# Kernel tuning notes

Measured on AMD Instinct MI355X. Metric: run time of the kernel, lower is better.

Reference implementation:

```python
import jax, jax.numpy as jnp
import numpy as np

N, IN, HID, H, OUT, G = 2048, 128, 128, 4, 10, 8
NEG_SLOPE = 0.2
THRESHOLD = 0.0


def setup_inputs() -> dict:
    key = jax.random.key(0)
    ks = jax.random.split(key, 18)
    s = 0.05
    return {
        "x": jax.random.normal(ks[0], (N, IN), jnp.float32),
        "attn_tensor": jax.random.normal(ks[1], (12, N, N), jnp.float32),
        "batch_idx": jnp.sort(jax.random.randint(ks[2], (N,), 0, G)),
        "conv_w": jax.random.normal(ks[3], (12,), jnp.float32) * s,
        "conv_b": jnp.zeros((), jnp.float32),
        "W1": jax.random.normal(ks[4], (IN, H * HID), jnp.float32) * s,
        "att_src1": jax.random.normal(ks[5], (H, HID), jnp.float32) * s,
        "att_dst1": jax.random.normal(ks[6], (H, HID), jnp.float32) * s,
        "att_edge1": jax.random.normal(ks[7], (H, HID), jnp.float32) * s,
        "We1": jax.random.normal(ks[8], (H * HID,), jnp.float32) * s,
        "b1": jnp.zeros((H * HID,), jnp.float32),
        "W2": jax.random.normal(ks[9], (H * HID, HID), jnp.float32) * s,
        "att_src2": jax.random.normal(ks[10], (1, HID), jnp.float32) * s,
        "att_dst2": jax.random.normal(ks[11], (1, HID), jnp.float32) * s,
        "att_edge2": jax.random.normal(ks[12], (1, HID), jnp.float32) * s,
        "We2": jax.random.normal(ks[13], (HID,), jnp.float32) * s,
        "b2": jnp.zeros((HID,), jnp.float32),
        "fc_w": jax.random.normal(ks[14], (HID, OUT), jnp.float32) * s,
        "fc_b": jnp.zeros((OUT,), jnp.float32),
    }


def gat_layer(x, adj, eattr, W, a_src, a_dst, a_edge, We, b, heads, out_ch):
    n = x.shape[0]
    h = (x @ W).reshape(n, heads, out_ch)            # [N,H,C]
    s_src = jnp.einsum('nhc,hc->nh', h, a_src)       # alpha contribution of source node
    s_dst = jnp.einsum('nhc,hc->nh', h, a_dst)       # alpha contribution of target node
    c_e = jnp.einsum('hc,hc->h', a_edge, We.reshape(heads, out_ch))  # scalar edge coeff per head
    # logits[s,t,h] for message s -> t (edge (s,t) means agg_mat[s,t] > thr)
    logits = s_src[:, None, :] + s_dst[None, :, :] + eattr[:, :, None] * c_e[None, None, :]
    logits = jnp.where(logits >= 0, logits, NEG_SLOPE * logits)  # leaky_relu(0.2)
    logits = jnp.where(adj[:, :, None], logits, -1e9)
    alpha = jax.nn.softmax(logits, axis=0)           # segment softmax over sources per target
    out = jnp.einsum('sth,shc->thc', alpha, h).reshape(n, heads * out_ch)
    return out + b


def reference(x, attn_tensor, batch_idx, conv_w, conv_b,
              W1, att_src1, att_dst1, att_edge1, We1, b1,
              W2, att_src2, att_dst2, att_edge2, We2, b2,
              fc_w, fc_b):
    # 1x1 conv over 12 attention channels -> dense [N,N] aggregated matrix
    agg = jnp.einsum('c,cst->st', conv_w, attn_tensor) + conv_b
    eye = jnp.eye(N, dtype=bool)
    mask_off = (agg > THRESHOLD) & (~eye)            # PyG GATConv removes then re-adds self loops
    # self-loop edge_attr = mean of incoming edge attrs per target (fill_value='mean')
    cnt = mask_off.sum(axis=0)
    mean_attr = jnp.where(mask_off, agg, 0.0).sum(axis=0) / jnp.maximum(cnt, 1)
    eattr = jnp.where(mask_off, agg, 0.0) + jnp.diag(mean_attr)
    adj = mask_off | eye

    h = gat_layer(x, adj, eattr, W1, att_src1, att_dst1, att_edge1, We1, b1, H, HID)
    h = jax.nn.relu(h)
    h = gat_layer(h, adj, eattr, W2, att_src2, att_dst2, att_edge2, We2, b2, 1, HID)

    sums = jax.ops.segment_sum(h, batch_idx, num_segments=G)
    counts = jax.ops.segment_sum(jnp.ones((N,), h.dtype), batch_idx, num_segments=G)
    pooled = sums / jnp.maximum(counts, 1.0)[:, None]  # global_mean_pool
    return jax.nn.log_softmax(pooled @ fc_w + fc_b, axis=1)
```

## Files before the change

### kernel.cpp

```cpp
#include <hip/hip_runtime.h>
#include <hip/hip_bf16.h>
#include <math.h>

#define NN 2048
#define NEG_SLOPE 0.2f

typedef __attribute__((ext_vector_type(8))) short bf16x8;
typedef __attribute__((ext_vector_type(4))) float f32x4;

static __device__ inline short f2bf(float x) {
  union { float f; unsigned u; } v;
  v.f = x;
  unsigned r = v.u + 0x7fffu + ((v.u >> 16) & 1u);
  return (short)(r >> 16);
}

__global__ __launch_bounds__(256) void k_pre(
    const float* __restrict__ attn, const float* __restrict__ conv_w,
    const float* __restrict__ conv_b, const float* __restrict__ W1,
    const float* __restrict__ W2, const float* __restrict__ ae1,
    const float* __restrict__ We1, const float* __restrict__ ae2,
    const float* __restrict__ We2, float* __restrict__ aggT,
    float* __restrict__ ssum_part, float* __restrict__ scnt_part,
    __hip_bfloat16* __restrict__ w1t, __hip_bfloat16* __restrict__ w2t,
    float* __restrict__ ce) {
  const int b = blockIdx.x;
  const int tid = threadIdx.x;
  if (b < 1024) {
    __shared__ float tile[64][68];
    const int t0 = (b & 31) * 64;
    const int s0 = (b >> 5) * 64;
    const int sl = tid >> 4;
    const int t4 = (tid & 15) * 4;
    float w[12];
#pragma unroll
    for (int c = 0; c < 12; ++c) w[c] = conv_w[c];
    const float cb = conv_b[0];
    f32x4 acc[4];
#pragma unroll
    for (int k = 0; k < 4; ++k) acc[k] = (f32x4){cb, cb, cb, cb};
    for (int c = 0; c < 12; ++c) {
      const float* base =
          attn + (size_t)c * NN * NN + (size_t)(s0 + sl) * NN + t0 + t4;
#pragma unroll
      for (int k = 0; k < 4; ++k)
        acc[k] += w[c] * *(const f32x4*)(base + (size_t)k * 16 * NN);
    }
#pragma unroll
    for (int k = 0; k < 4; ++k) *(f32x4*)&tile[sl + 16 * k][t4] = acc[k];
    __syncthreads();
    const int tl = tid >> 2;
    const int sq = (tid & 3) * 16;
    const int tglob = t0 + tl;
    float* orow = aggT + (size_t)tglob * NN + s0 + sq;
    float psum = 0.f, pcnt = 0.f;
#pragma unroll
    for (int g = 0; g < 4; ++g) {
      f32x4 v = {tile[sq + 4 * g][tl], tile[sq + 4 * g + 1][tl],
                 tile[sq + 4 * g + 2][tl], tile[sq + 4 * g + 3][tl]};
      *(f32x4*)(orow + 4 * g) = v;
#pragma unroll
      for (int j = 0; j < 4; ++j) {
        int sglob = s0 + sq + 4 * g + j;
        bool m = (v[j] > 0.f) && (sglob != tglob);
        psum += m ? v[j] : 0.f;
        pcnt += m ? 1.f : 0.f;
      }
    }
    psum += __shfl_down(psum, 1); psum += __shfl_down(psum, 2);
    pcnt += __shfl_down(pcnt, 1); pcnt += __shfl_down(pcnt, 2);
    if ((tid & 3) == 0) {
      ssum_part[(b >> 5) * NN + tglob] = psum;
      scnt_part[(b >> 5) * NN + tglob] = pcnt;
    }
  } else if (b < 1056) {
#pragma unroll
    for (int k = 0; k < 8; ++k) {
      int o = (b - 1024) * 2048 + k * 256 + tid;
      ((short*)w1t)[o] = f2bf(W1[(o & 127) * 512 + (o >> 7)]);
    }
  } else if (b < 1088) {
#pragma unroll
    for (int k = 0; k < 8; ++k) {
      int o = (b - 1056) * 2048 + k * 256 + tid;
      ((short*)w2t)[o] = f2bf(W2[(o & 511) * 128 + (o >> 9)]);
    }
  } else {
    const int lane = tid & 63;
    const int wv = tid >> 6;
    float q1 = ae1[wv * 128 + lane] * We1[wv * 128 + lane] +
               ae1[wv * 128 + 64 + lane] * We1[wv * 128 + 64 + lane];
    for (int off = 32; off; off >>= 1) q1 += __shfl_down(q1, off);
    if (lane == 0) ce[wv] = q1;
    float q2 = ae2[lane] * We2[lane] + ae2[64 + lane] * We2[64 + lane];
    for (int off = 32; off; off >>= 1) q2 += __shfl_down(q2, off);
    if (tid == 0) ce[4] = q2;
  }
}

__global__ __launch_bounds__(256) void k_gemm1(
    const float* __restrict__ x, const __hip_bfloat16* __restrict__ w1t,
    const float* __restrict__ asrc1, const float* __restrict__ adst1,
    __hip_bfloat16* __restrict__ hTsw1, float* __restrict__ sspart1,
    float* __restrict__ sdpart1) {
  const int tid = threadIdx.x;
  const int w = (int)blockIdx.x * 4 + (tid >> 6);
  const int lane = tid & 63, row = lane & 15, kg = lane >> 4;
  const int mb = w >> 4, nb = w & 15;
  const int m0 = mb * 16, n0 = nb * 32;
  const float* axrow = x + (size_t)(m0 + row) * 128 + kg * 8;
  f32x4 acc[2];
#pragma unroll
  for (int f = 0; f < 2; ++f) acc[f] = (f32x4){0.f, 0.f, 0.f, 0.f};
#pragma unroll
  for (int ks = 0; ks < 4; ++ks) {
    f32x4 xa = *(const f32x4*)(axrow + ks * 32);
    f32x4 xb = *(const f32x4*)(axrow + ks * 32 + 4);
    bf16x8 Af = {f2bf(xa[0]), f2bf(xa[1]), f2bf(xa[2]), f2bf(xa[3]),
                 f2bf(xb[0]), f2bf(xb[1]), f2bf(xb[2]), f2bf(xb[3])};
#pragma unroll
    for (int f = 0; f < 2; ++f) {
      bf16x8 Bf = *(const bf16x8*)(w1t + (size_t)(n0 + f * 16 + row) * 128 +
                                   kg * 8 + ks * 32);
      acc[f] = __builtin_amdgcn_mfma_f32_16x16x32_bf16(Af, Bf, acc[f], 0, 0, 0);
    }
  }
  const int h = nb >> 2;
  float as[2], ad[2];
#pragma unroll
  for (int f = 0; f < 2; ++f) {
    int ch = (n0 + f * 16 + row) & 127;
    as[f] = asrc1[h * 128 + ch];
    ad[f] = adst1[h * 128 + ch];
  }
  float ps[4] = {0.f, 0.f, 0.f, 0.f}, pd[4] = {0.f, 0.f, 0.f, 0.f};
#pragma unroll
  for (int f = 0; f < 2; ++f)
#pragma unroll
    for (int r = 0; r < 4; ++r) {
      ps[r] += acc[f][r] * as[f];
      pd[r] += acc[f][r] * ad[f];
    }
#pragma unroll
  for (int m = 1; m < 16; m <<= 1) {
#pragma unroll
    for (int r = 0; r < 4; ++r) {
      ps[r] += __shfl_xor(ps[r], m);
      pd[r] += __shfl_xor(pd[r], m);
    }
  }
  if (row == 0) {
#pragma unroll
    for (int r = 0; r < 4; ++r) {
      int node = m0 + kg * 4 + r;
      sspart1[nb * NN + node] = ps[r];
      sdpart1[nb * NN + node] = pd[r];
    }
  }
#pragma unroll
  for (int f = 0; f < 2; ++f) {
    const int cbi = nb * 2 + f;
    short4 ct;
    ct.x = f2bf(acc[f][0]); ct.y = f2bf(acc[f][1]);
    ct.z = f2bf(acc[f][2]); ct.w = f2bf(acc[f][3]);
    size_t a4 = (size_t)cbi * (NN * 16) +
                (size_t)(((m0 >> 3) + (kg >> 1)) * 128 + row * 8 + (kg & 1) * 4);
    *(short4*)((short*)hTsw1 + a4) = ct;
  }
}

__global__ __launch_bounds__(256) void k_attn1(
    const float* __restrict__ aggT, const __hip_bfloat16* __restrict__ hTsw1,
    const float* __restrict__ sspart1, const float* __restrict__ sdpart1,
    const float* __restrict__ ssum_part, const float* __restrict__ scnt_part,
    const float* __restrict__ ce_all, const float* __restrict__ b1,
    __hip_bfloat16* __restrict__ feat1b) {
  const int tid = threadIdx.x;
  const int t0 = (int)(blockIdx.x >> 2) * 16;
  const int h = (int)(blockIdx.x & 3u);
  __shared__ float ss_sh[2048];
  __shared__ float red[4][16][128];
  __shared__ float den_sh[4][16];
  for (int i = tid; i < 2048; i += 256)
    ss_sh[i] = sspart1[(4 * h + 0) * NN + i] + sspart1[(4 * h + 1) * NN + i] +
               sspart1[(4 * h + 2) * NN + i] + sspart1[(4 * h + 3) * NN + i];
  __syncthreads();
  const int lane = tid & 63, w = tid >> 6, row = lane & 15, kg = lane >> 4;
  const int sbeg = w * 512;
  const int tRow = t0 + row;
  const float* arow = aggT + (size_t)tRow * NN;
  float msum = 0.f, mcnt = 0.f;
#pragma unroll
  for (int q = 0; q < 32; ++q) {
    msum += ssum_part[q * NN + tRow];
    mcnt += scnt_part[q * NN + tRow];
  }
  const float ma_t = msum / fmaxf(mcnt, 1.f);
  const float ce = ce_all[h];
  const float sd_t = sdpart1[(4 * h + 0) * NN + tRow] +
                     sdpart1[(4 * h + 1) * NN + tRow] +
                     sdpart1[(4 * h + 2) * NN + tRow] +
                     sdpart1[(4 * h + 3) * NN + tRow];
  const float* ssh = ss_sh + sbeg;
  const __hip_bfloat16* bbase =
      hTsw1 + (size_t)(h * 8) * (NN * 16) + kg * 128 + row * 8;
  f32x4 acc[8];
#pragma unroll
  for (int f = 0; f < 8; ++f) acc[f] = (f32x4){0.f, 0.f, 0.f, 0.f};
  float dpart = 0.f;
  for (int s0 = sbeg; s0 < sbeg + 512; s0 += 32) {
    const int sk = s0 + kg * 8;
    f32x4 a0 = *(const f32x4*)(arow + sk);
    f32x4 a1 = *(const f32x4*)(arow + sk + 4);
    f32x4 sv0 = *(const f32x4*)(ssh + (sk - sbeg));
    f32x4 sv1 = *(const f32x4*)(ssh + (sk - sbeg) + 4);
    float av[8] = {a0[0], a0[1], a0[2], a0[3], a1[0], a1[1], a1[2], a1[3]};
    float sv[8] = {sv0[0], sv0[1], sv0[2], sv0[3],
                   sv1[0], sv1[1], sv1[2], sv1[3]};
    short pb[8];
#pragma unroll
    for (int j = 0; j < 8; ++j) {
      const int s = sk + j;
      const float a = av[j];
      const bool diag = (s == tRow);
      const float ev = diag ? ma_t : a;
      const bool adj = diag || (a > 0.f);
      float l = sv[j] + sd_t + ev * ce;
      l = fmaxf(l, NEG_SLOPE * l);
      const float pv = adj ? __expf(l) : 0.f;
      dpart += pv;
      pb[j] = f2bf(pv);
    }
    bf16x8 A = {pb[0], pb[1], pb[2], pb[3], pb[4], pb[5], pb[6], pb[7]};
    const __hip_bfloat16* bp = bbase + (size_t)s0 * 16;
#pragma unroll
    for (int f = 0; f < 8; ++f) {
      bf16x8 B = *(const bf16x8*)(bp + (size_t)f * (NN * 16));
      acc[f] = __builtin_amdgcn_mfma_f32_16x16x32_bf16(A, B, acc[f], 0, 0, 0);
    }
  }
  dpart += __shfl_xor(dpart, 16);
  dpart += __shfl_xor(dpart, 32);
  __syncthreads();
#pragma unroll
  for (int f = 0; f < 8; ++f)
#pragma unroll
    for (int r = 0; r < 4; ++r) red[w][kg * 4 + r][f * 16 + row] = acc[f][r];
  if (lane < 16) den_sh[w][lane] = dpart;
  __syncthreads();
#pragma unroll
  for (int i = 0; i < 8; ++i) {
    int idx = i * 256 + tid;
    int t = idx >> 7, c = idx & 127;
    float nsum = red[0][t][c] + red[1][t][c] + red[2][t][c] + red[3][t][c];
    float dsum = den_sh[0][t] + den_sh[1][t] + den_sh[2][t] + den_sh[3][t];
    float v = nsum / dsum + b1[h * 128 + c];
    feat1b[(size_t)(t0 + t) * 512 + h * 128 + c] =
        __float2bfloat16(v > 0.f ? v : 0.f);
  }
}

__global__ __launch_bounds__(256) void k_gemm2(
    const __hip_bfloat16* __restrict__ feat1b,
    const __hip_bfloat16* __restrict__ w2t, const float* __restrict__ asrc2,
    const float* __restrict__ adst2, __hip_bfloat16* __restrict__ hTsw2,
    float* __restrict__ ssrc2, float* __restrict__ sdst2) {
  const int tid = threadIdx.x;
  const int wv = tid >> 6;
  const int w = (int)blockIdx.x * 4 + wv;
  const int lane = tid & 63, row = lane & 15, kg = lane >> 4;
  const int mb = w >> 2, nb = w & 3;
  const int m0 = mb * 16, n0 = nb * 32;
  __shared__ float sred[2][4][16];
  const __hip_bfloat16* arow = feat1b + (size_t)(m0 + row) * 512 + kg * 8;
  f32x4 acc[2];
#pragma unroll
  for (int f = 0; f < 2; ++f) acc[f] = (f32x4){0.f, 0.f, 0.f, 0.f};
#pragma unroll
  for (int ks = 0; ks < 16; ++ks) {
    bf16x8 Af = *(const bf16x8*)(arow + ks * 32);
#pragma unroll
    for (int f = 0; f < 2; ++f) {
      bf16x8 Bf = *(const bf16x8*)(w2t + (size_t)(n0 + f * 16 + row) * 512 +
                                   kg * 8 + ks * 32);
      acc[f] = __builtin_amdgcn_mfma_f32_16x16x32_bf16(Af, Bf, acc[f], 0, 0, 0);
    }
  }
  float as[2], ad[2];
#pragma unroll
  for (int f = 0; f < 2; ++f) {
    int ch = (n0 + f * 16 + row) & 127;
    as[f] = asrc2[ch];
    ad[f] = adst2[ch];
  }
  float ps[4] = {0.f, 0.f, 0.f, 0.f}, pd[4] = {0.f, 0.f, 0.f, 0.f};
#pragma unroll
  for (int f = 0; f < 2; ++f)
#pragma unroll
    for (int r = 0; r < 4; ++r) {
      ps[r] += acc[f][r] * as[f];
      pd[r] += acc[f][r] * ad[f];
    }
#pragma unroll
  for (int m = 1; m < 16; m <<= 1) {
#pragma unroll
    for (int r = 0; r < 4; ++r) {
      ps[r] += __shfl_xor(ps[r], m);
      pd[r] += __shfl_xor(pd[r], m);
    }
  }
  if (row == 0) {
#pragma unroll
    for (int r = 0; r < 4; ++r) {
      sred[0][wv][kg * 4 + r] = ps[r];
      sred[1][wv][kg * 4 + r] = pd[r];
    }
  }
  __syncthreads();
  if (tid < 16) {
    float s = sred[0][0][tid] + sred[0][1][tid] + sred[0][2][tid] +
              sred[0][3][tid];
    float d = sred[1][0][tid] + sred[1][1][tid] + sred[1][2][tid] +
              sred[1][3][tid];
    ssrc2[(int)blockIdx.x * 16 + tid] = s;
    sdst2[(int)blockIdx.x * 16 + tid] = d;
  }
#pragma unroll
  for (int f = 0; f < 2; ++f) {
    const int cbi = nb * 2 + f;
    short4 ct;
    ct.x = f2bf(acc[f][0]); ct.y = f2bf(acc[f][1]);
    ct.z = f2bf(acc[f][2]); ct.w = f2bf(acc[f][3]);
    size_t a4 = (size_t)cbi * (NN * 16) +
                (size_t)(((m0 >> 3) + (kg >> 1)) * 128 + row * 8 + (kg & 1) * 4);
    *(short4*)((short*)hTsw2 + a4) = ct;
  }
}

__global__ __launch_bounds__(256) void k_attn2(
    const float* __restrict__ aggT, const __hip_bfloat16* __restrict__ hTsw2,
    const float* __restrict__ ssrc2, const float* __restrict__ sdst2,
    const float* __restrict__ ssum_part, const float* __restrict__ scnt_part,
    const float* __restrict__ ce_all, const float* __restrict__ b2,
    float* __restrict__ feat2) {
  const int tid = threadIdx.x;
  const int t0 = (int)(blockIdx.x >> 1) * 16;
  const int chalf = (int)(blockIdx.x & 1u);
  __shared__ float ss_sh[2048];
  __shared__ float red[4][16][64];
  __shared__ float den_sh[4][16];
  for (int i = tid; i < 2048; i += 256) ss_sh[i] = ssrc2[i];
  __syncthreads();
  const int lane = tid & 63, w = tid >> 6, row = lane & 15, kg = lane >> 4;
  const int sbeg = w * 512;
  const int tRow = t0 + row;
  const float* arow = aggT + (size_t)tRow * NN;
  float msum = 0.f, mcnt = 0.f;
#pragma unroll
  for (int q = 0; q < 32; ++q) {
    msum += ssum_part[q * NN + tRow];
    mcnt += scnt_part[q * NN + tRow];
  }
  const float ma_t = msum / fmaxf(mcnt, 1.f);
  const float ce = ce_all[4];
  const float sd_t = sdst2[tRow];
  const float* ssh = ss_sh + sbeg;
  const __hip_bfloat16* bbase =
      hTsw2 + (size_t)(chalf * 4) * (NN * 16) + kg * 128 + row * 8;
  f32x4 acc[4];
#pragma unroll
  for (int f = 0; f < 4; ++f) acc[f] = (f32x4){0.f, 0.f, 0.f, 0.f};
  float dpart = 0.f;
  for (int s0 = sbeg; s0 < sbeg + 512; s0 += 32) {
    const int sk = s0 + kg * 8;
    f32x4 a0 = *(const f32x4*)(arow + sk);
    f32x4 a1 = *(const f32x4*)(arow + sk + 4);
    f32x4 sv0 = *(const f32x4*)(ssh + (sk - sbeg));
    f32x4 sv1 = *(const f32x4*)(ssh + (sk - sbeg) + 4);
    float av[8] = {a0[0], a0[1], a0[2], a0[3], a1[0], a1[1], a1[2], a1[3]};
    float sv[8] = {sv0[0], sv0[1], sv0[2], sv0[3],
                   sv1[0], sv1[1], sv1[2], sv1[3]};
    short pb[8];
#pragma unroll
    for (int j = 0; j < 8; ++j) {
      const int s = sk + j;
      const float a = av[j];
      const bool diag = (s == tRow);
      const float ev = diag ? ma_t : a;
      const bool adj = diag || (a > 0.f);
      float l = sv[j] + sd_t + ev * ce;
      l = fmaxf(l, NEG_SLOPE * l);
      const float pv = adj ? __expf(l) : 0.f;
      dpart += pv;
      pb[j] = f2bf(pv);
    }
    bf16x8 A = {pb[0], pb[1], pb[2], pb[3], pb[4], pb[5], pb[6], pb[7]};
    const __hip_bfloat16* bp = bbase + (size_t)s0 * 16;
#pragma unroll
    for (int f = 0; f < 4; ++f) {
      bf16x8 B = *(const bf16x8*)(bp + (size_t)f * (NN * 16));
      acc[f] = __builtin_amdgcn_mfma_f32_16x16x32_bf16(A, B, acc[f], 0, 0, 0);
    }
  }
  dpart += __shfl_xor(dpart, 16);
  dpart += __shfl_xor(dpart, 32);
  __syncthreads();
#pragma unroll
  for (int f = 0; f < 4; ++f)
#pragma unroll
    for (int r = 0; r < 4; ++r) red[w][kg * 4 + r][f * 16 + row] = acc[f][r];
  if (lane < 16) den_sh[w][lane] = dpart;
  __syncthreads();
#pragma unroll
  for (int i = 0; i < 4; ++i) {
    int idx = i * 256 + tid;
    int t = idx >> 6, c = idx & 63;
    float nsum = red[0][t][c] + red[1][t][c] + red[2][t][c] + red[3][t][c];
    float dsum = den_sh[0][t] + den_sh[1][t] + den_sh[2][t] + den_sh[3][t];
    feat2[(size_t)(t0 + t) * 128 + chalf * 64 + c] =
        nsum / dsum + b2[chalf * 64 + c];
  }
}

__global__ __launch_bounds__(256) void k_poolhead(
    const float* __restrict__ feat, const int* __restrict__ bidx,
    const float* __restrict__ fcw, const float* __restrict__ fcb,
    float* __restrict__ out) {
  const int g = blockIdx.x;
  const int tid = threadIdx.x;
  __shared__ int lo[2];
  __shared__ float ps2[256];
  __shared__ float lsh[10];
  if (tid == 0) { lo[0] = NN; lo[1] = NN; }
  __syncthreads();
  for (int n = tid; n < NN; n += 256) {
    int b = bidx[n];
    int bprev = (n == 0) ? -1 : bidx[n - 1];
    if (b >= g && bprev < g) atomicMin(&lo[0], n);
    if (b >= g + 1 && bprev < g + 1) atomicMin(&lo[1], n);
  }
  __syncthreads();
  int s = lo[0], e = lo[1];
  const int c = tid & 127, half = tid >> 7;
  float sum = 0.f;
  for (int n = s + half; n < e; n += 2) sum += feat[(size_t)n * 128 + c];
  ps2[tid] = sum;
  __syncthreads();
  if (tid < 128) {
    float cntf = (float)((e - s) > 1 ? (e - s) : 1);
    ps2[tid] = (ps2[tid] + ps2[tid + 128]) / cntf;
  }
  __syncthreads();
  if (tid < 10) {
    float v = fcb[tid];
    for (int ch = 0; ch < 128; ++ch) v += ps2[ch] * fcw[ch * 10 + tid];
    lsh[tid] = v;
  }
  __syncthreads();
  if (tid < 10) {
    float m = -1e30f;
    for (int i = 0; i < 10; ++i) m = fmaxf(m, lsh[i]);
    float den = 0.f;
    for (int i = 0; i < 10; ++i) den += expf(lsh[i] - m);
    out[g * 10 + tid] = lsh[tid] - m - logf(den);
  }
}

extern "C" void kernel_launch(void* const* d_in, const int* in_sizes, int n_in,
                              void* d_out, int out_size, void* d_ws,
                              size_t ws_size, hipStream_t stream) {
  (void)in_sizes; (void)n_in; (void)out_size; (void)ws_size;
  const float* x      = (const float*)d_in[0];
  const float* attn   = (const float*)d_in[1];
  const int*   bidx   = (const int*)d_in[2];
  const float* conv_w = (const float*)d_in[3];
  const float* conv_b = (const float*)d_in[4];
  const float* W1     = (const float*)d_in[5];
  const float* asrc1  = (const float*)d_in[6];
  const float* adst1  = (const float*)d_in[7];
  const float* aedge1 = (const float*)d_in[8];
  const float* We1    = (const float*)d_in[9];
  const float* b1     = (const float*)d_in[10];
  const float* W2     = (const float*)d_in[11];
  const float* asrc2  = (const float*)d_in[12];
  const float* adst2  = (const float*)d_in[13];
  const float* aedge2 = (const float*)d_in[14];
  const float* We2    = (const float*)d_in[15];
  const float* b2     = (const float*)d_in[16];
  const float* fcw    = (const float*)d_in[17];
  const float* fcb    = (const float*)d_in[18];

  float* ws = (float*)d_ws;
  float* aggT      = ws;
  float* feat2     = aggT + 4194304;
  float* ssum_part = feat2 + 262144;
  float* scnt_part = ssum_part + 65536;
  float* sspart1   = scnt_part + 65536;
  float* sdpart1   = sspart1 + 32768;
  float* ssrc2     = sdpart1 + 32768;
  float* sdst2     = ssrc2 + 2048;
  float* ce        = sdst2 + 2048;
  float* bf        = ce + 64;
  __hip_bfloat16* w1t    = (__hip_bfloat16*)bf;
  __hip_bfloat16* w2t    = (__hip_bfloat16*)(bf + 32768);
  __hip_bfloat16* hTsw1  = (__hip_bfloat16*)(bf + 65536);
  __hip_bfloat16* hTsw2  = (__hip_bfloat16*)(bf + 589824);
  __hip_bfloat16* feat1b = (__hip_bfloat16*)(bf + 720896);

  k_pre<<<1089, 256, 0, stream>>>(attn, conv_w, conv_b, W1, W2, aedge1, We1,
                                  aedge2, We2, aggT, ssum_part, scnt_part, w1t,
                                  w2t, ce);
  k_gemm1<<<512, 256, 0, stream>>>(x, w1t, asrc1, adst1, hTsw1, sspart1,
                                   sdpart1);
  k_attn1<<<512, 256, 0, stream>>>(aggT, hTsw1, sspart1, sdpart1, ssum_part,
                                   scnt_part, ce, b1, feat1b);
  k_gemm2<<<128, 256, 0, stream>>>(feat1b, w2t, asrc2, adst2, hTsw2, ssrc2,
                                   sdst2);
  k_attn2<<<256, 256, 0, stream>>>(aggT, hTsw2, ssrc2, sdst2, ssum_part,
                                   scnt_part, ce, b2, feat2);
  k_poolhead<<<8, 256, 0, stream>>>(feat2, bidx, fcw, fcb, (float*)d_out);
}
```

Measured before the change: 133.3 us.

## Fuse layer-1 GEMM into preprocessing kernel with in-LDS W1 transpose

```diff
diff --git a/kernel.cpp b/kernel.cpp
--- a/kernel.cpp
+++ b/kernel.cpp
@@ -17,19 +17,100 @@
 
 __global__ __launch_bounds__(256) void k_pre(
     const float* __restrict__ attn, const float* __restrict__ conv_w,
-    const float* __restrict__ conv_b, const float* __restrict__ W1,
-    const float* __restrict__ W2, const float* __restrict__ ae1,
-    const float* __restrict__ We1, const float* __restrict__ ae2,
-    const float* __restrict__ We2, float* __restrict__ aggT,
-    float* __restrict__ ssum_part, float* __restrict__ scnt_part,
-    __hip_bfloat16* __restrict__ w1t, __hip_bfloat16* __restrict__ w2t,
-    float* __restrict__ ce) {
+    const float* __restrict__ conv_b, const float* __restrict__ x,
+    const float* __restrict__ W1, const float* __restrict__ W2,
+    const float* __restrict__ asrc1, const float* __restrict__ adst1,
+    const float* __restrict__ ae1, const float* __restrict__ We1,
+    const float* __restrict__ ae2, const float* __restrict__ We2,
+    float* __restrict__ aggT, float* __restrict__ ssum_part,
+    float* __restrict__ scnt_part, __hip_bfloat16* __restrict__ hTsw1,
+    float* __restrict__ sspart1, float* __restrict__ sdpart1,
+    __hip_bfloat16* __restrict__ w2t, float* __restrict__ ce) {
   const int b = blockIdx.x;
   const int tid = threadIdx.x;
-  if (b < 1024) {
-    __shared__ float tile[64][68];
-    const int t0 = (b & 31) * 64;
-    const int s0 = (b >> 5) * 64;
+  __shared__ __align__(16) char smem[34816];
+  if (b < 512) {
+    typedef short w1row[136];
+    w1row* w1s = (w1row*)smem;
+    const int mb = b >> 2, cblk = b & 3;
+    const int m0 = mb * 16;
+    for (int e = tid; e < 128 * 32; e += 256) {
+      int k = e >> 5, cq = (e & 31) * 4;
+      f32x4 v = *(const f32x4*)(W1 + (size_t)k * 512 + cblk * 128 + cq);
+#pragma unroll
+      for (int j = 0; j < 4; ++j) w1s[cq + j][k] = f2bf(v[j]);
+    }
+    __syncthreads();
+    const int wv = tid >> 6;
+    const int lane = tid & 63, row = lane & 15, kg = lane >> 4;
+    const int nb = cblk * 4 + wv;
+    const int n0l = wv * 32;
+    const float* axrow = x + (size_t)(m0 + row) * 128 + kg * 8;
+    f32x4 acc[2];
+#pragma unroll
+    for (int f = 0; f < 2; ++f) acc[f] = (f32x4){0.f, 0.f, 0.f, 0.f};
+#pragma unroll
+    for (int ks = 0; ks < 4; ++ks) {
+      f32x4 xa = *(const f32x4*)(axrow + ks * 32);
+      f32x4 xb = *(const f32x4*)(axrow + ks * 32 + 4);
+      bf16x8 Af = {f2bf(xa[0]), f2bf(xa[1]), f2bf(xa[2]), f2bf(xa[3]),
+                   f2bf(xb[0]), f2bf(xb[1]), f2bf(xb[2]), f2bf(xb[3])};
+#pragma unroll
+      for (int f = 0; f < 2; ++f) {
+        bf16x8 Bf = *(const bf16x8*)&w1s[n0l + f * 16 + row][kg * 8 + ks * 32];
+        acc[f] =
+            __builtin_amdgcn_mfma_f32_16x16x32_bf16(Af, Bf, acc[f], 0, 0, 0);
+      }
+    }
+    const int h = nb >> 2;
+    float as[2], ad[2];
+#pragma unroll
+    for (int f = 0; f < 2; ++f) {
+      int ch = (n0l + f * 16 + row) & 127;
+      as[f] = asrc1[h * 128 + ch];
+      ad[f] = adst1[h * 128 + ch];
+    }
+    float ps[4] = {0.f, 0.f, 0.f, 0.f}, pd[4] = {0.f, 0.f, 0.f, 0.f};
+#pragma unroll
+    for (int f = 0; f < 2; ++f)
+#pragma unroll
+      for (int r = 0; r < 4; ++r) {
+        ps[r] += acc[f][r] * as[f];
+        pd[r] += acc[f][r] * ad[f];
+      }
+#pragma unroll
+    for (int m = 1; m < 16; m <<= 1) {
+#pragma unroll
+      for (int r = 0; r < 4; ++r) {
+        ps[r] += __shfl_xor(ps[r], m);
+        pd[r] += __shfl_xor(pd[r], m);
+      }
+    }
+    if (row == 0) {
+#pragma unroll
+      for (int r = 0; r < 4; ++r) {
+        int node = m0 + kg * 4 + r;
+        sspart1[nb * NN + node] = ps[r];
+        sdpart1[nb * NN + node] = pd[r];
+      }
+    }
+#pragma unroll
+    for (int f = 0; f < 2; ++f) {
+      const int cbi = nb * 2 + f;
+      short4 ct;
+      ct.x = f2bf(acc[f][0]); ct.y = f2bf(acc[f][1]);
+      ct.z = f2bf(acc[f][2]); ct.w = f2bf(acc[f][3]);
+      size_t a4 =
+          (size_t)cbi * (NN * 16) +
+          (size_t)(((m0 >> 3) + (kg >> 1)) * 128 + row * 8 + (kg & 1) * 4);
+      *(short4*)((short*)hTsw1 + a4) = ct;
+    }
+  } else if (b < 1536) {
+    typedef float trow[68];
+    trow* tile = (trow*)smem;
+    const int b2 = b - 512;
+    const int t0 = (b2 & 31) * 64;
+    const int s0 = (b2 >> 5) * 64;
     const int sl = tid >> 4;
     const int t4 = (tid & 15) * 4;
     float w[12];
@@ -70,19 +151,13 @@
     psum += __shfl_down(psum, 1); psum += __shfl_down(psum, 2);
     pcnt += __shfl_down(pcnt, 1); pcnt += __shfl_down(pcnt, 2);
     if ((tid & 3) == 0) {
-      ssum_part[(b >> 5) * NN + tglob] = psum;
-      scnt_part[(b >> 5) * NN + tglob] = pcnt;
-    }
-  } else if (b < 1056) {
+      ssum_part[(b2 >> 5) * NN + tglob] = psum;
+      scnt_part[(b2 >> 5) * NN + tglob] = pcnt;
+    }
+  } else if (b < 1568) {
 #pragma unroll
     for (int k = 0; k < 8; ++k) {
-      int o = (b - 1024) * 2048 + k * 256 + tid;
-      ((short*)w1t)[o] = f2bf(W1[(o & 127) * 512 + (o >> 7)]);
-    }
-  } else if (b < 1088) {
-#pragma unroll
-    for (int k = 0; k < 8; ++k) {
-      int o = (b - 1056) * 2048 + k * 256 + tid;
+      int o = (b - 1536) * 2048 + k * 256 + tid;
       ((short*)w2t)[o] = f2bf(W2[(o & 511) * 128 + (o >> 9)]);
     }
   } else {
@@ -95,77 +170,6 @@
     float q2 = ae2[lane] * We2[lane] + ae2[64 + lane] * We2[64 + lane];
     for (int off = 32; off; off >>= 1) q2 += __shfl_down(q2, off);
     if (tid == 0) ce[4] = q2;
-  }
-}
-
-__global__ __launch_bounds__(256) void k_gemm1(
-    const float* __restrict__ x, const __hip_bfloat16* __restrict__ w1t,
-    const float* __restrict__ asrc1, const float* __restrict__ adst1,
-    __hip_bfloat16* __restrict__ hTsw1, float* __restrict__ sspart1,
-    float* __restrict__ sdpart1) {
-  const int tid = threadIdx.x;
-  const int w = (int)blockIdx.x * 4 + (tid >> 6);
-  const int lane = tid & 63, row = lane & 15, kg = lane >> 4;
-  const int mb = w >> 4, nb = w & 15;
-  const int m0 = mb * 16, n0 = nb * 32;
-  const float* axrow = x + (size_t)(m0 + row) * 128 + kg * 8;
-  f32x4 acc[2];
-#pragma unroll
-  for (int f = 0; f < 2; ++f) acc[f] = (f32x4){0.f, 0.f, 0.f, 0.f};
-#pragma unroll
-  for (int ks = 0; ks < 4; ++ks) {
-    f32x4 xa = *(const f32x4*)(axrow + ks * 32);
-    f32x4 xb = *(const f32x4*)(axrow + ks * 32 + 4);
-    bf16x8 Af = {f2bf(xa[0]), f2bf(xa[1]), f2bf(xa[2]), f2bf(xa[3]),
-                 f2bf(xb[0]), f2bf(xb[1]), f2bf(xb[2]), f2bf(xb[3])};
-#pragma unroll
-    for (int f = 0; f < 2; ++f) {
-      bf16x8 Bf = *(const bf16x8*)(w1t + (size_t)(n0 + f * 16 + row) * 128 +
-                                   kg * 8 + ks * 32);
-      acc[f] = __builtin_amdgcn_mfma_f32_16x16x32_bf16(Af, Bf, acc[f], 0, 0, 0);
-    }
-  }
-  const int h = nb >> 2;
-  float as[2], ad[2];
-#pragma unroll
-  for (int f = 0; f < 2; ++f) {
-    int ch = (n0 + f * 16 + row) & 127;
-    as[f] = asrc1[h * 128 + ch];
-    ad[f] = adst1[h * 128 + ch];
-  }
-  float ps[4] = {0.f, 0.f, 0.f, 0.f}, pd[4] = {0.f, 0.f, 0.f, 0.f};
-#pragma unroll
-  for (int f = 0; f < 2; ++f)
-#pragma unroll
-    for (int r = 0; r < 4; ++r) {
-      ps[r] += acc[f][r] * as[f];
-      pd[r] += acc[f][r] * ad[f];
-    }
-#pragma unroll
-  for (int m = 1; m < 16; m <<= 1) {
-#pragma unroll
-    for (int r = 0; r < 4; ++r) {
-      ps[r] += __shfl_xor(ps[r], m);
-      pd[r] += __shfl_xor(pd[r], m);
-    }
-  }
-  if (row == 0) {
-#pragma unroll
-    for (int r = 0; r < 4; ++r) {
-      int node = m0 + kg * 4 + r;
-      sspart1[nb * NN + node] = ps[r];
-      sdpart1[nb * NN + node] = pd[r];
-    }
-  }
-#pragma unroll
-  for (int f = 0; f < 2; ++f) {
-    const int cbi = nb * 2 + f;
-    short4 ct;
-    ct.x = f2bf(acc[f][0]); ct.y = f2bf(acc[f][1]);
-    ct.z = f2bf(acc[f][2]); ct.w = f2bf(acc[f][3]);
-    size_t a4 = (size_t)cbi * (NN * 16) +
-                (size_t)(((m0 >> 3) + (kg >> 1)) * 128 + row * 8 + (kg & 1) * 4);
-    *(short4*)((short*)hTsw1 + a4) = ct;
   }
 }
 
@@ -501,17 +505,15 @@
   float* sdst2     = ssrc2 + 2048;
   float* ce        = sdst2 + 2048;
   float* bf        = ce + 64;
-  __hip_bfloat16* w1t    = (__hip_bfloat16*)bf;
-  __hip_bfloat16* w2t    = (__hip_bfloat16*)(bf + 32768);
-  __hip_bfloat16* hTsw1  = (__hip_bfloat16*)(bf + 65536);
-  __hip_bfloat16* hTsw2  = (__hip_bfloat16*)(bf + 589824);
-  __hip_bfloat16* feat1b = (__hip_bfloat16*)(bf + 720896);
-
-  k_pre<<<1089, 256, 0, stream>>>(attn, conv_w, conv_b, W1, W2, aedge1, We1,
-                                  aedge2, We2, aggT, ssum_part, scnt_part, w1t,
-                                  w2t, ce);
-  k_gemm1<<<512, 256, 0, stream>>>(x, w1t, asrc1, adst1, hTsw1, sspart1,
-                                   sdpart1);
+  __hip_bfloat16* w2t    = (__hip_bfloat16*)bf;
+  __hip_bfloat16* hTsw1  = (__hip_bfloat16*)(bf + 32768);
+  __hip_bfloat16* hTsw2  = (__hip_bfloat16*)(bf + 557056);
+  __hip_bfloat16* feat1b = (__hip_bfloat16*)(bf + 688128);
+
+  k_pre<<<1569, 256, 0, stream>>>(attn, conv_w, conv_b, x, W1, W2, asrc1,
+                                  adst1, aedge1, We1, aedge2, We2, aggT,
+                                  ssum_part, scnt_part, hTsw1, sspart1,
+                                  sdpart1, w2t, ce);
   k_attn1<<<512, 256, 0, stream>>>(aggT, hTsw1, sspart1, sdpart1, ssum_part,
                                    scnt_part, ce, b1, feat1b);
   k_gemm2<<<128, 256, 0, stream>>>(feat1b, w2t, asrc2, adst2, hTsw2, ssrc2,
```

Measured after the change: 131.8 us. No clear change (-1.1%).
